# Performance work log

Hardware: AMD Instinct MI355X
Metric: run time of the kernel (lower is better)

The kernel has to match this reference:

```python
import jax, jax.numpy as jnp
import numpy as np

B, D, H, S, E = 16384, 512, 1024, 8, 4
DH = D // 2  # attention hidden


def setup_inputs() -> dict:
    key = jax.random.key(0)
    ks = jax.random.split(key, 20)
    std = 0.1
    return {
        "x": jax.random.normal(ks[0], (B, D), jnp.float32),
        "scenario_ids": jax.random.randint(ks[1], (B,), 0, S, jnp.int32),
        # shared SEI gate
        "gate_w": jax.random.normal(ks[2], (D, E), jnp.float32) * std,
        "gate_b": jnp.zeros((E,), jnp.float32),
        # shared sub-experts (stacked): D -> H -> D
        "sub_w1": jax.random.normal(ks[3], (E, D, H), jnp.float32) * std,
        "sub_b1": jnp.zeros((E, H), jnp.float32),
        "sub_w2": jax.random.normal(ks[4], (E, H, D), jnp.float32) * std,
        "sub_b2": jnp.zeros((E, D), jnp.float32),
        # scenario-specific experts (stacked): D -> H -> D
        "spec_w1": jax.random.normal(ks[5], (S, D, H), jnp.float32) * std,
        "spec_b1": jnp.zeros((S, H), jnp.float32),
        "spec_w2": jax.random.normal(ks[6], (S, H, D), jnp.float32) * std,
        "spec_b2": jnp.zeros((S, D), jnp.float32),
        # SAN scenario embeddings + attention MLP (2D -> D/2 -> 1)
        "scen_embed": jax.random.normal(ks[7], (S, D), jnp.float32) * std,
        "attn_w1": jax.random.normal(ks[8], (2 * D, DH), jnp.float32) * std,
        "attn_b1": jnp.zeros((DH,), jnp.float32),
        "attn_w2": jax.random.normal(ks[9], (DH, 1), jnp.float32) * std,
        "attn_b2": jnp.zeros((1,), jnp.float32),
        # SAN output projection (4D -> D)
        "out_w": jax.random.normal(ks[10], (4 * D, D), jnp.float32) * std,
        "out_b": jnp.zeros((D,), jnp.float32),
    }


def reference(x, scenario_ids, gate_w, gate_b, sub_w1, sub_b1, sub_w2, sub_b2,
              spec_w1, spec_b1, spec_w2, spec_b2, scen_embed,
              attn_w1, attn_b1, attn_w2, attn_b2, out_w, out_b):
    b = x.shape[0]
    # --- shared expert (SEI): softmax-gated mixture of E sub-experts ---
    gates = jax.nn.softmax(x @ gate_w + gate_b, axis=-1)            # [B,E]
    h = jax.nn.relu(jnp.einsum('bd,edh->ebh', x, sub_w1) + sub_b1[:, None, :])
    exp_out = jnp.einsum('ebh,ehd->ebd', h, sub_w2) + sub_b2[:, None, :]
    shared = jnp.einsum('be,ebd->bd', gates, exp_out)               # [B,D]
    # --- scenario-specific experts: run all, gather per-sample ---
    hs = jax.nn.relu(jnp.einsum('bd,sdh->sbh', x, spec_w1) + spec_b1[:, None, :])
    spec_all = jnp.einsum('sbh,shd->sbd', hs, spec_w2) + spec_b2[:, None, :]  # [S,B,D]
    specific = spec_all[scenario_ids, jnp.arange(b)]                # [B,D]
    # --- scenario-aware attention (SAN) ---
    # logits[s,b] = MLP(cat([shared[b], scen_embed[s]]))
    s = scen_embed.shape[0]
    comb = jnp.concatenate([
        jnp.broadcast_to(shared[None], (s, b, shared.shape[-1])),
        jnp.broadcast_to(scen_embed[:, None, :], (s, b, scen_embed.shape[-1])),
    ], axis=-1)                                                      # [S,B,2D]
    ah = jax.nn.relu(comb @ attn_w1 + attn_b1)                       # [S,B,D/2]
    logits = (ah @ attn_w2 + attn_b2)[..., 0]                        # [S,B]
    attn_w = jax.nn.softmax(logits.T, axis=-1)                       # [B,S]
    # in the original, all non-current scenario reprs are zeros, so the
    # weighted sums reduce to w[b, sid[b]] * (shared/specific)
    wsel = jnp.take_along_axis(attn_w, scenario_ids[:, None], axis=1)  # [B,1]
    enhanced = jnp.concatenate([shared, wsel * shared, specific, wsel * specific], axis=-1)
    return enhanced @ out_w + out_b                                  # [B,D]
```

## Files before the change

### kernel.cpp

```cpp
#include <hip/hip_runtime.h>
#include <hip/hip_bf16.h>
#include <stdint.h>

typedef __hip_bfloat16 bf16;
typedef __attribute__((ext_vector_type(8))) short short8;
typedef __attribute__((ext_vector_type(4))) short short4v;
typedef __attribute__((ext_vector_type(4))) float f32x4;

constexpr int cB = 16384, cD = 512, cH = 1024, cS = 8, cE = 4, cDH = 256;

__device__ __forceinline__ float tof(bf16 v) { return __bfloat162float(v); }
__device__ __forceinline__ bf16 tob(float v) { return __float2bfloat16(v); }
__device__ __forceinline__ float b2f(short s) {
  uint32_t u = ((uint32_t)(uint16_t)s) << 16;
  return __builtin_bit_cast(float, u);
}
__device__ __forceinline__ float ldf(const void* p, long i, int isbf) {
  return isbf ? b2f(((const short*)p)[i]) : ((const float*)p)[i];
}
__device__ __forceinline__ void stbf_nt(bf16* p, float v) {
  __builtin_nontemporal_store(__builtin_bit_cast(short, tob(v)), (short*)p);
}

__device__ __forceinline__ void gload_lds16(const bf16* g, char* l) {
  __builtin_amdgcn_global_load_lds(
      (const __attribute__((address_space(1))) void*)g,
      (__attribute__((address_space(3))) void*)l, 16, 0, 0);
}

__global__ __launch_bounds__(256) void probe_k(const void* x, int* flag) {
  __shared__ int sh[256];
  const unsigned short* u = (const unsigned short*)x;
  int cnt = 0;
  for (int i = threadIdx.x; i < 2048; i += 256) {
    float v = fabsf(b2f((short)u[2 * i]));
    cnt += (v > 1e-5f && v < 1e3f) ? 1 : 0;
  }
  sh[threadIdx.x] = cnt;
  __syncthreads();
  for (int s = 128; s > 0; s >>= 1) {
    if (threadIdx.x < s) sh[threadIdx.x] += sh[threadIdx.x + s];
    __syncthreads();
  }
  if (threadIdx.x == 0) flag[0] = (sh[0] > 1024) ? 1 : 0;
}

__global__ __launch_bounds__(256) void cvtx_k(const void* x, bf16* xb, const int* flag) {
  int g = blockIdx.x * 256 + threadIdx.x;
  if (flag[0]) {
    ((short8*)xb)[g] = ((const short8*)x)[g];
  } else {
    const f32x4* xf = (const f32x4*)x;
    f32x4 v0 = xf[2 * g], v1 = xf[2 * g + 1];
    short8 o;
#pragma unroll
    for (int j = 0; j < 4; j++) {
      o[j] = __builtin_bit_cast(short, tob(v0[j]));
      o[j + 4] = __builtin_bit_cast(short, tob(v1[j]));
    }
    ((short8*)xb)[g] = o;
  }
}

struct CvtDesc {
  const void* src[11];
  int off[12];
};
__global__ __launch_bounds__(256) void cvt_smalls_k(CvtDesc d, const int* flag, float* dst) {
  int i = blockIdx.x * 256 + threadIdx.x;
  if (i >= d.off[11]) return;
  int isb = flag[0];
  int j = 0;
  while (i >= d.off[j + 1]) j++;
  dst[i] = ldf(d.src[j], i - d.off[j], isb);
}

__global__ __launch_bounds__(256) void transpose_k(const void* in, bf16* out, int ldin, int ldout,
                                                   long in_off, long in_bs, long out_bs,
                                                   const int* flag) {
  __shared__ float tile[32][33];
  int isb = flag[0];
  long src0 = in_off + (long)blockIdx.z * in_bs;
  bf16* dst = out + (long)blockIdx.z * out_bs;
  int c0 = blockIdx.x * 32, r0 = blockIdx.y * 32;
  int tx = threadIdx.x & 31, ty = threadIdx.x >> 5;
#pragma unroll
  for (int i = 0; i < 4; i++)
    tile[ty + i * 8][tx] = ldf(in, src0 + (long)(r0 + ty + i * 8) * ldin + c0 + tx, isb);
  __syncthreads();
#pragma unroll
  for (int i = 0; i < 4; i++)
    dst[(long)(c0 + ty + i * 8) * ldout + r0 + tx] = tob(tile[tx][ty + i * 8]);
}

__global__ __launch_bounds__(256) void owt_k(const void* ow, bf16* owpair, const int* flag) {
  __shared__ float tile[32][33];
  int isb = flag[0];
  int z = blockIdx.z;
  int m = z & 1, kb = (z >> 1) * 512;
  long base = (long)z * 512 * cD;
  int c0 = blockIdx.x * 32, r0 = blockIdx.y * 32;
  int tx = threadIdx.x & 31, ty = threadIdx.x >> 5;
#pragma unroll
  for (int i = 0; i < 4; i++)
    tile[ty + i * 8][tx] = ldf(ow, base + (long)(r0 + ty + i * 8) * cD + c0 + tx, isb);
  __syncthreads();
#pragma unroll
  for (int i = 0; i < 4; i++) {
    int n = c0 + ty + i * 8;
    int R = ((n >> 6) << 7) + (((n >> 5) & 1) << 6) + (m << 5) + (((n >> 4) & 1) << 4) + (n & 15);
    owpair[(long)R * 1024 + kb + r0 + tx] = tob(tile[tx][ty + i * 8]);
  }
}

struct GArgs {
  const bf16* A; int lda;
  const bf16* Bt; int ldb; long bt_stride;
  void* C; int ldc;
  int M, N, K;
  const float* bias; int bias_stride;
  const float* gates; int eidx;
  const int* perm; const int* cum;
  const float* wsel;
  const int* dflag;
};

template <int EPI, bool GROUPED, bool GATHER_A, bool SCATTER_C, bool SPLITK = false>
__global__ __launch_bounds__(256, 4) void gemm_k(GArgs a) {
  __shared__ char smem[32768];
  char* ldsA = smem;
  char* ldsB = smem + 16384;

  int bxs, bys;
  if constexpr (!GROUPED) {
    const int gx = gridDim.x;
    const int nwg = gx * gridDim.y;
    const int d = blockIdx.y * gx + blockIdx.x;
    const int q = nwg >> 3, r = nwg & 7;
    const int xcd = d & 7, di = d >> 3;
    const int logical = (xcd < r ? xcd * (q + 1) : r * (q + 1) + (xcd - r) * q) + di;
    bxs = logical % gx;
    bys = logical / gx;
  } else {
    bxs = blockIdx.x;
    bys = blockIdx.y;
  }

  int g0, cnt;
  if constexpr (GROUPED) {
    int z = blockIdx.z;
    g0 = a.cum[z];
    cnt = a.cum[z + 1] - g0;
  } else {
    g0 = 0;
    cnt = a.M;
  }
  const int ptile = bys * 128;
  if (ptile >= cnt) return;
  const int n0 = bxs * 128;
  const int zk = SPLITK ? blockIdx.z * a.K : 0;
  const int zc = SPLITK ? blockIdx.z * a.eidx : 0;

  const int t = threadIdx.x, w = t >> 6, l = t & 63;
  const int wm = w >> 1, wn = w & 1;

  const bf16* bt = a.Bt + (GROUPED ? (long)blockIdx.z * a.bt_stride : 0);
  const float* bias = a.bias ? (a.bias + (GROUPED ? blockIdx.z * a.bias_stride : 0)) : nullptr;

  const bf16* aSrc[4];
  const bf16* bSrc[4];
  int ldsOff[4];
#pragma unroll
  for (int c = 0; c < 4; c++) {
    int pos = w * 4096 + c * 1024 + l * 16;
    int row = pos >> 7;
    int su = ((((pos >> 4) & 7) ^ (row & 7))) * 8;
    int p = ptile + row;
    if (p > cnt - 1) p = cnt - 1;
    int ar;
    if constexpr (GATHER_A) ar = a.perm[g0 + p];
    else ar = g0 + p;
    aSrc[c] = a.A + (long)ar * a.lda + zk + su;
    bSrc[c] = bt + (long)(n0 + row) * a.ldb + zk + su;
    ldsOff[c] = w * 4096 + c * 1024;
  }

  f32x4 zero = {0.f, 0.f, 0.f, 0.f};
  f32x4 acc[4][4];
#pragma unroll
  for (int i = 0; i < 4; i++)
#pragma unroll
    for (int j = 0; j < 4; j++) acc[i][j] = zero;

  const int nkt = a.K >> 6;
  for (int kt = 0; kt < nkt; ++kt) {
#pragma unroll
    for (int c = 0; c < 4; c++) gload_lds16(aSrc[c] + kt * 64, ldsA + ldsOff[c]);
#pragma unroll
    for (int c = 0; c < 4; c++) gload_lds16(bSrc[c] + kt * 64, ldsB + ldsOff[c]);
    __syncthreads();
#pragma unroll
    for (int kk = 0; kk < 2; kk++) {
      short8 af[4], bv[4];
#pragma unroll
      for (int mi = 0; mi < 4; mi++) {
        int row = wm * 64 + mi * 16 + (l & 15);
        int kg = kk * 4 + (l >> 4);
        int off = row * 128 + ((kg ^ (row & 7)) << 4);
        af[mi] = *(const short8*)(ldsA + off);
      }
#pragma unroll
      for (int ni = 0; ni < 4; ni++) {
        int row = wn * 64 + ni * 16 + (l & 15);
        int kg = kk * 4 + (l >> 4);
        int off = row * 128 + ((kg ^ (row & 7)) << 4);
        bv[ni] = *(const short8*)(ldsB + off);
      }
#pragma unroll
      for (int mi = 0; mi < 4; mi++)
#pragma unroll
        for (int ni = 0; ni < 4; ni++)
          acc[mi][ni] =
              __builtin_amdgcn_mfma_f32_16x16x32_bf16(af[mi], bv[ni], acc[mi][ni], 0, 0, 0);
    }
    __syncthreads();
  }

  const int l15 = l & 15, lg4 = l >> 4;
  int outbf = 1;
  if constexpr (EPI == 9) outbf = a.dflag[0];
#pragma unroll
  for (int mi = 0; mi < 4; mi++) {
#pragma unroll
    for (int j = 0; j < 4; j++) {
      int p = ptile + wm * 64 + mi * 16 + lg4 * 4 + j;
      if (p >= cnt) continue;
      int crow;
      if constexpr (SCATTER_C) crow = a.perm[g0 + p];
      else crow = g0 + p;
      if constexpr (EPI == 9) {
        float wv = a.wsel[crow];
#pragma unroll
        for (int ni = 0; ni < 2; ni++) {
          int n = (n0 >> 1) + wn * 32 + ni * 16 + l15;
          float o = acc[mi][ni][j] + wv * acc[mi][ni + 2][j] + a.bias[n];
          if (outbf) ((bf16*)a.C)[(long)crow * a.ldc + n] = tob(o);
          else ((float*)a.C)[(long)crow * a.ldc + n] = o;
        }
        continue;
      }
#pragma unroll
      for (int ni = 0; ni < 4; ni++) {
        int n = n0 + wn * 64 + ni * 16 + l15;
        float v = acc[mi][ni][j];
        if constexpr (EPI == 1) {
          v += bias[n];
          v = fmaxf(v, 0.f);
          stbf_nt(&((bf16*)a.C)[(long)crow * a.ldc + n], v);
        } else if constexpr (EPI == 2) {
          float g = a.gates[(long)(g0 + p) * 4 + a.eidx];
          v = g * (v + bias[n]);
          float* Cf = (float*)a.C;
          long idx = (long)crow * a.ldc + n;
          if (a.eidx == 0) Cf[idx] = v;
          else Cf[idx] += v;
        } else if constexpr (EPI == 3) {
          ((float*)a.C)[(long)crow * a.ldc + n] = v;
        } else if constexpr (EPI == 4) {
          v += bias[n];
          ((bf16*)a.C)[(long)crow * a.ldc + n] = tob(v);
        } else if constexpr (EPI == 6) {
          float g = a.gates[(long)(g0 + p) * 4 + (n >> 10)];
          v = g * fmaxf(v + bias[n], 0.f);
          stbf_nt(&((bf16*)a.C)[(long)crow * a.ldc + n], v);
        } else if constexpr (EPI == 7) {
          const float* gr = a.gates + (long)(g0 + p) * 4;
          v += gr[0] * bias[n] + gr[1] * bias[512 + n] + gr[2] * bias[1024 + n] +
               gr[3] * bias[1536 + n];
          ((bf16*)a.C)[(long)crow * a.ldc + n] = tob(v);
        } else if constexpr (EPI == 8) {
          ((bf16*)a.C)[(long)crow * a.ldc + n + zc] = tob(v);
        }
      }
    }
  }
}

__global__ __launch_bounds__(256) void combine_k(bf16* ss, const float* gates, const float* sb2) {
  long i = (long)blockIdx.x * 256 + threadIdx.x;
  int r = (int)(i >> 6);
  int c8 = (int)(i & 63) * 8;
  short8 p0 = *(const short8*)(ss + (long)r * 1024 + c8);
  short8 p1 = *(const short8*)(ss + (long)r * 1024 + 512 + c8);
  const float* gr = gates + (long)r * 4;
  float g0 = gr[0], g1 = gr[1], g2 = gr[2], g3 = gr[3];
  short8 o;
#pragma unroll
  for (int j = 0; j < 8; j++) {
    int c = c8 + j;
    float v = b2f(p0[j]) + b2f(p1[j]) + g0 * sb2[c] + g1 * sb2[512 + c] + g2 * sb2[1024 + c] +
              g3 * sb2[1536 + c];
    o[j] = __builtin_bit_cast(short, tob(v));
  }
  *(short8*)(ss + (long)r * 1024 + c8) = o;
}

__global__ __launch_bounds__(256) void gates_k(const bf16* x, const float* gw, const float* gb,
                                               float* gates) {
  int b = blockIdx.x * 4 + (threadIdx.x >> 6);
  int l = threadIdx.x & 63;
  short8 xv = *(const short8*)(x + (long)b * cD + l * 8);
  float a0 = 0, a1 = 0, a2 = 0, a3 = 0;
#pragma unroll
  for (int j = 0; j < 8; j++) {
    float xf = b2f(xv[j]);
    f32x4 wr = *(const f32x4*)(gw + (l * 8 + j) * 4);
    a0 += xf * wr[0];
    a1 += xf * wr[1];
    a2 += xf * wr[2];
    a3 += xf * wr[3];
  }
#pragma unroll
  for (int o = 32; o > 0; o >>= 1) {
    a0 += __shfl_xor(a0, o);
    a1 += __shfl_xor(a1, o);
    a2 += __shfl_xor(a2, o);
    a3 += __shfl_xor(a3, o);
  }
  a0 += gb[0];
  a1 += gb[1];
  a2 += gb[2];
  a3 += gb[3];
  float m = fmaxf(fmaxf(a0, a1), fmaxf(a2, a3));
  float e0 = expf(a0 - m), e1 = expf(a1 - m), e2 = expf(a2 - m), e3 = expf(a3 - m);
  float s = e0 + e1 + e2 + e3;
  if (l == 0) {
    float* gp = gates + (long)b * 4;
    gp[0] = e0 / s;
    gp[1] = e1 / s;
    gp[2] = e2 / s;
    gp[3] = e3 / s;
  }
}

__global__ __launch_bounds__(256) void bhist_k(const int* sid, int* bh) {
  int blk = blockIdx.x, t = threadIdx.x;
  __shared__ int h[cS];
  if (t < cS) h[t] = 0;
  __syncthreads();
  int s = sid[blk * 256 + t];
#pragma unroll
  for (int q = 0; q < cS; q++) {
    unsigned long long m = __ballot(s == q);
    if ((t & 63) == 0) atomicAdd(&h[q], __popcll(m));
  }
  __syncthreads();
  if (t < cS) bh[blk * cS + t] = h[t];
}

__global__ void bbase_k(const int* bh, int* base, int* cum) {
  __shared__ int tot[cS];
  int s = threadIdx.x;
  if (s < cS) {
    int run = 0;
    for (int b = 0; b < 64; b++) {
      base[b * cS + s] = run;
      run += bh[b * cS + s];
    }
    tot[s] = run;
  }
  __syncthreads();
  if (s == 0) {
    int run = 0;
    for (int q = 0; q < cS; q++) {
      cum[q] = run;
      run += tot[q];
    }
    cum[cS] = run;
  }
  __syncthreads();
  if (s < cS) {
    int c = cum[s];
    for (int b = 0; b < 64; b++) base[b * cS + s] += c;
  }
}

__global__ __launch_bounds__(256) void bscat_k(const int* sid, const int* base, int* perm) {
  int blk = blockIdx.x, t = threadIdx.x, w = t >> 6, l = t & 63;
  __shared__ int wc[4][cS];
  __shared__ int wb[4][cS];
  int s = sid[blk * 256 + t];
  int rank = 0;
#pragma unroll
  for (int q = 0; q < cS; q++) {
    unsigned long long m = __ballot(s == q);
    if (l == 0) wc[w][q] = __popcll(m);
    if (s == q) rank = __popcll(m & ((1ull << l) - 1ull));
  }
  __syncthreads();
  if (t < cS) {
    int run = 0;
#pragma unroll
    for (int ww = 0; ww < 4; ww++) {
      wb[ww][t] = run;
      run += wc[ww][t];
    }
  }
  __syncthreads();
  perm[base[blk * cS + s] + wb[w][s] + rank] = blk * 256 + t;
}

__global__ __launch_bounds__(256) void scenpart_k(const float* emb, const float* w1,
                                                  const float* b1, float* scp) {
  __shared__ float red[8][32];
  int s = blockIdx.x;
  int nl = threadIdx.x & 31;
  int n = blockIdx.y * 32 + nl;
  int dg = threadIdx.x >> 5;
  float a = 0.f;
#pragma unroll 4
  for (int d = dg * 64; d < dg * 64 + 64; d++) a += emb[s * cD + d] * w1[(long)(cD + d) * cDH + n];
  red[dg][nl] = a;
  __syncthreads();
  if (dg == 0) {
    float t = b1[n];
#pragma unroll
    for (int g = 0; g < 8; g++) t += red[g][nl];
    scp[s * cDH + n] = t;
  }
}

__global__ __launch_bounds__(256) void wsel_k(const float* sp, const float* scp, const float* w2,
                                              const int* sid, float* wsel) {
  int b = blockIdx.x * 4 + (threadIdx.x >> 6);
  int l = threadIdx.x & 63;
  float spv[4], w2v[4];
#pragma unroll
  for (int q = 0; q < 4; q++) {
    spv[q] = sp[(long)b * cDH + q * 64 + l];
    w2v[q] = w2[q * 64 + l];
  }
  float lg[8];
#pragma unroll
  for (int s = 0; s < 8; s++) {
    float acc = 0.f;
#pragma unroll
    for (int q = 0; q < 4; q++) {
      float v = spv[q] + scp[s * cDH + q * 64 + l];
      v = fmaxf(v, 0.f);
      acc += v * w2v[q];
    }
#pragma unroll
    for (int o = 32; o > 0; o >>= 1) acc += __shfl_xor(acc, o);
    lg[s] = acc;
  }
  float m = lg[0];
#pragma unroll
  for (int s = 1; s < 8; s++) m = fmaxf(m, lg[s]);
  float sum = 0.f;
#pragma unroll
  for (int s = 0; s < 8; s++) sum += expf(lg[s] - m);
  if (l == 0) {
    int s0 = sid[b];
    wsel[b] = expf(lg[s0] - m) / sum;
  }
}

__global__ __launch_bounds__(256) void cvt_shared_k(const float* sf, bf16* ss) {
  int i = blockIdx.x * 256 + threadIdx.x;
  int r = i >> 7, c = (i & 127) * 4;
  f32x4 v = *(const f32x4*)(sf + (long)r * cD + c);
  short4v o;
#pragma unroll
  for (int j = 0; j < 4; j++) o[j] = __builtin_bit_cast(short, tob(v[j]));
  *(short4v*)(ss + (long)r * 1024 + c) = o;
}

extern "C" void kernel_launch(void* const* d_in, const int* in_sizes, int n_in, void* d_out,
                              int out_size, void* d_ws, size_t ws_size, hipStream_t stream) {
  const void* x = d_in[0];
  const int* sid = (const int*)d_in[1];

  char* ws = (char*)d_ws;
  size_t off = 0;
  auto alloc = [&](size_t bytes) -> void* {
    void* p = ws + off;
    off += (bytes + 255) & ~(size_t)255;
    return p;
  };
  int* g_flag = (int*)alloc(64);
  float* g_gates = (float*)alloc((size_t)cB * 4 * 4);
  float* g_wsel = (float*)alloc((size_t)cB * 4);
  int* g_perm = (int*)alloc((size_t)cB * 4);
  int* g_bh = (int*)alloc(64 * cS * 4);
  int* g_base = (int*)alloc(64 * cS * 4);
  int* g_cum = (int*)alloc(64);
  float* g_scp = (float*)alloc((size_t)cS * cDH * 4);
  float* g_small = (float*)alloc((size_t)300000 * 4);
  bf16* g_xb = (bf16*)alloc((size_t)cB * cD * 2);
  bf16* w1t = (bf16*)alloc((size_t)cE * cH * cD * 2);
  bf16* w2cat = (bf16*)alloc((size_t)cD * 4096 * 2);
  bf16* s1t = (bf16*)alloc((size_t)cS * cH * cD * 2);
  bf16* s2t = (bf16*)alloc((size_t)cS * cD * cH * 2);
  bf16* a1t = (bf16*)alloc((size_t)cDH * cD * 2);
  bf16* owpair = (bf16*)alloc((size_t)1024 * 1024 * 2);
  bf16* g_ss = (bf16*)alloc((size_t)cB * 1024 * 2);
  size_t fixed_end = off;
  const size_t MB = 1024ull * 1024ull;
  const bool BIG = (ws_size == 0) || (fixed_end + 135 * MB <= ws_size);
  char* g_big = (char*)alloc(BIG ? 135 * MB : 68 * MB);
  (void)in_sizes;
  (void)n_in;
  (void)out_size;

  dim3 blk(256);
  probe_k<<<1, blk, 0, stream>>>(x, g_flag);
  cvtx_k<<<cB * cD / 8 / 256, blk, 0, stream>>>(x, g_xb, g_flag);

  const int O_GW = 0, O_GB = 2048, O_SB1 = 2052, O_SB2 = 6148, O_PB1 = 8196, O_PB2 = 16388,
            O_EMB = 20484, O_AW1 = 24580, O_AB1 = 286724, O_AW2 = 286980, O_OB = 287236,
            O_END = 287748;
  {
    CvtDesc d;
    const void* srcs[11] = {d_in[2],  d_in[3],  d_in[5],  d_in[7],  d_in[9], d_in[11],
                            d_in[12], d_in[13], d_in[14], d_in[15], d_in[18]};
    int offs[12] = {O_GW, O_GB, O_SB1, O_SB2, O_PB1, O_PB2, O_EMB, O_AW1, O_AB1, O_AW2, O_OB,
                    O_END};
    for (int i = 0; i < 11; i++) d.src[i] = srcs[i];
    for (int i = 0; i < 12; i++) d.off[i] = offs[i];
    cvt_smalls_k<<<(O_END + 255) / 256, blk, 0, stream>>>(d, g_flag, g_small);
  }

  transpose_k<<<dim3(cH / 32, cD / 32, cE), blk, 0, stream>>>(d_in[4], w1t, cH, cD, 0,
                                                              (long)cD * cH, (long)cH * cD, g_flag);
  transpose_k<<<dim3(cD / 32, cH / 32, cE), blk, 0, stream>>>(d_in[6], w2cat, cD, 4096, 0,
                                                              (long)cH * cD, 1024, g_flag);
  transpose_k<<<dim3(cH / 32, cD / 32, cS), blk, 0, stream>>>(d_in[8], s1t, cH, cD, 0,
                                                              (long)cD * cH, (long)cH * cD, g_flag);
  transpose_k<<<dim3(cD / 32, cH / 32, cS), blk, 0, stream>>>(d_in[10], s2t, cD, cH, 0,
                                                              (long)cH * cD, (long)cD * cH, g_flag);
  transpose_k<<<dim3(cDH / 32, cD / 32, 1), blk, 0, stream>>>(d_in[13], a1t, cDH, cD, 0, 0, 0,
                                                              g_flag);
  owt_k<<<dim3(cD / 32, cD / 32, 4), blk, 0, stream>>>(d_in[17], owpair, g_flag);

  gates_k<<<cB / 4, blk, 0, stream>>>(g_xb, g_small + O_GW, g_small + O_GB, g_gates);
  bhist_k<<<cB / 256, blk, 0, stream>>>(sid, g_bh);
  bbase_k<<<1, 64, 0, stream>>>(g_bh, g_base, g_cum);
  bscat_k<<<cB / 256, blk, 0, stream>>>(sid, g_base, g_perm);

  if (BIG) {
    bf16* h4 = (bf16*)g_big;
    float* sp = (float*)g_big;
    bf16* hspec = (bf16*)g_big;
    {
      GArgs a{};
      a.A = g_xb; a.lda = cD; a.Bt = w1t; a.ldb = cD;
      a.C = h4; a.ldc = 4096; a.M = cB; a.N = 4096; a.K = cD;
      a.bias = g_small + O_SB1; a.gates = g_gates;
      gemm_k<6, false, false, false><<<dim3(32, cB / 128), blk, 0, stream>>>(a);
    }
    {
      GArgs a{};
      a.A = h4; a.lda = 4096; a.Bt = w2cat; a.ldb = 4096;
      a.C = g_ss; a.ldc = 1024; a.M = cB; a.N = cD; a.K = 2048;
      a.eidx = 512;
      gemm_k<8, false, false, false, true><<<dim3(cD / 128, cB / 128, 2), blk, 0, stream>>>(a);
    }
    combine_k<<<cB * 64 / 256, blk, 0, stream>>>(g_ss, g_gates, g_small + O_SB2);
    {
      GArgs a{};
      a.A = g_ss; a.lda = 1024; a.Bt = a1t; a.ldb = cD;
      a.C = sp; a.ldc = cDH; a.M = cB; a.N = cDH; a.K = cD;
      gemm_k<3, false, false, false><<<dim3(cDH / 128, cB / 128), blk, 0, stream>>>(a);
    }
    scenpart_k<<<dim3(cS, 8), blk, 0, stream>>>(g_small + O_EMB, g_small + O_AW1, g_small + O_AB1,
                                                g_scp);
    wsel_k<<<cB / 4, blk, 0, stream>>>(sp, g_scp, g_small + O_AW2, sid, g_wsel);
    {
      GArgs a{};
      a.A = g_xb; a.lda = cD; a.Bt = s1t; a.ldb = cD; a.bt_stride = (long)cH * cD;
      a.C = hspec; a.ldc = cH; a.M = cB; a.N = cH; a.K = cD;
      a.bias = g_small + O_PB1; a.bias_stride = cH;
      a.perm = g_perm; a.cum = g_cum;
      gemm_k<1, true, true, false><<<dim3(cH / 128, cB / 128, cS), blk, 0, stream>>>(a);
    }
    {
      GArgs a{};
      a.A = hspec; a.lda = cH; a.Bt = s2t; a.ldb = cH; a.bt_stride = (long)cD * cH;
      a.C = g_ss + 512; a.ldc = 1024; a.M = cB; a.N = cD; a.K = cH;
      a.bias = g_small + O_PB2; a.bias_stride = cD;
      a.perm = g_perm; a.cum = g_cum;
      gemm_k<4, true, false, true><<<dim3(cD / 128, cB / 128, cS), blk, 0, stream>>>(a);
    }
    {
      GArgs a{};
      a.A = g_ss; a.lda = 1024; a.Bt = owpair; a.ldb = 1024;
      a.C = d_out; a.ldc = cD; a.M = cB; a.N = 1024; a.K = 1024;
      a.bias = g_small + O_OB; a.wsel = g_wsel; a.dflag = g_flag;
      gemm_k<9, false, false, false><<<dim3(8, cB / 128), blk, 0, stream>>>(a);
    }
  } else {
    float* f32a = (float*)g_big;
    bf16* hbuf = (bf16*)(g_big + 34 * MB);
    for (int e = 0; e < cE; e++) {
      GArgs a1{};
      a1.A = g_xb; a1.lda = cD; a1.Bt = w1t + (size_t)e * cH * cD; a1.ldb = cD;
      a1.C = hbuf; a1.ldc = cH; a1.M = cB; a1.N = cH; a1.K = cD;
      a1.bias = g_small + O_SB1 + e * cH;
      gemm_k<1, false, false, false><<<dim3(cH / 128, cB / 128), blk, 0, stream>>>(a1);
      GArgs a2{};
      a2.A = hbuf; a2.lda = cH; a2.Bt = w2cat + (size_t)e * 1024; a2.ldb = 4096;
      a2.C = f32a; a2.ldc = cD; a2.M = cB; a2.N = cD; a2.K = cH;
      a2.bias = g_small + O_SB2 + e * cD; a2.gates = g_gates; a2.eidx = e;
      gemm_k<2, false, false, false><<<dim3(cD / 128, cB / 128), blk, 0, stream>>>(a2);
    }
    cvt_shared_k<<<cB * 128 / 256, blk, 0, stream>>>(f32a, g_ss);
    {
      GArgs a{};
      a.A = g_xb; a.lda = cD; a.Bt = s1t; a.ldb = cD; a.bt_stride = (long)cH * cD;
      a.C = hbuf; a.ldc = cH; a.M = cB; a.N = cH; a.K = cD;
      a.bias = g_small + O_PB1; a.bias_stride = cH;
      a.perm = g_perm; a.cum = g_cum;
      gemm_k<1, true, true, false><<<dim3(cH / 128, cB / 128, cS), blk, 0, stream>>>(a);
    }
    {
      GArgs a{};
      a.A = hbuf; a.lda = cH; a.Bt = s2t; a.ldb = cH; a.bt_stride = (long)cD * cH;
      a.C = g_ss + 512; a.ldc = 1024; a.M = cB; a.N = cD; a.K = cH;
      a.bias = g_small + O_PB2; a.bias_stride = cD;
      a.perm = g_perm; a.cum = g_cum;
      gemm_k<4, true, false, true><<<dim3(cD / 128, cB / 128, cS), blk, 0, stream>>>(a);
    }
    {
      GArgs a{};
      a.A = g_ss; a.lda = 1024; a.Bt = a1t; a.ldb = cD;
      a.C = f32a; a.ldc = cDH; a.M = cB; a.N = cDH; a.K = cD;
      gemm_k<3, false, false, false><<<dim3(cDH / 128, cB / 128), blk, 0, stream>>>(a);
    }
    scenpart_k<<<dim3(cS, 8), blk, 0, stream>>>(g_small + O_EMB, g_small + O_AW1, g_small + O_AB1,
                                                g_scp);
    wsel_k<<<cB / 4, blk, 0, stream>>>(f32a, g_scp, g_small + O_AW2, sid, g_wsel);
    {
      GArgs a{};
      a.A = g_ss; a.lda = 1024; a.Bt = owpair; a.ldb = 1024;
      a.C = d_out; a.ldc = cD; a.M = cB; a.N = 1024; a.K = 1024;
      a.bias = g_small + O_OB; a.wsel = g_wsel; a.dflag = g_flag;
      gemm_k<9, false, false, false><<<dim3(8, cB / 128), blk, 0, stream>>>(a);
    }
  }
}
```

Before: 419.1 us.

## Add 256x256-tile 8-wave GEMM kernel for the three large dense GEMMs

Adds a new GEMM kernel with 256x256 output tiles, 512 threads, 128 KB of double-buffered swizzled LDS, an XCD-aware block remap, and global loads interleaved between four MFMA phases using setprio and barriers. It replaces the 128x128 gemm_k for the shared-expert up-projection, the down-projection and the output projection. The intent is more operand reuse per tile, less global/L2 traffic, and better overlap of loads with MFMA. In exchange, occupancy drops to one workgroup per CU, and the grid gets small for the down-projection (256 blocks) and the output projection.

New measurement: 405.9 us. 3.2% less time.

```diff
diff --git a/kernel.cpp b/kernel.cpp
--- a/kernel.cpp
+++ b/kernel.cpp
@@ -286,6 +286,202 @@
   }
 }
 
+struct G6Args {
+  const bf16* A; int lda;
+  const bf16* Bt; int ldb;
+  void* C; int ldc;
+  int N, K;
+  const float* bias;
+  const float* gates;
+  const float* wsel;
+  const int* dflag;
+};
+
+template <int EPI>
+__global__ __launch_bounds__(512, 1) void g256_k(G6Args a) {
+  extern __shared__ char sm[];
+  const int t = threadIdx.x, w = t >> 6, l = t & 63;
+  const int wm = w >> 2, wn = w & 3;
+
+  const int gx = gridDim.x, nwg = gx * gridDim.y;
+  const int dd = blockIdx.y * gx + blockIdx.x;
+  const int q = nwg >> 3, r = nwg & 7;
+  const int xcd = dd & 7, di = dd >> 3;
+  const int logical = (xcd < r ? xcd * (q + 1) : r * (q + 1) + (xcd - r) * q) + di;
+  const int m0 = (logical / gx) * 256, n0 = (logical % gx) * 256;
+  const long zk = (long)blockIdx.z * a.K;
+
+  const bf16* srcP[8];
+  int ldsO[8];
+#pragma unroll
+  for (int c = 0; c < 8; c++) {
+    int pos = (c & 3) * 8192 + t * 16;
+    int row = pos >> 7;
+    int su = (((pos >> 4) & 7) ^ (row & 7)) * 8;
+    if (c < 4) {
+      srcP[c] = a.A + (long)(m0 + row) * a.lda + zk + su;
+      ldsO[c] = (c & 3) * 8192 + w * 1024;
+    } else {
+      srcP[c] = a.Bt + (long)(n0 + row) * a.ldb + zk + su;
+      ldsO[c] = 32768 + (c & 3) * 8192 + w * 1024;
+    }
+  }
+
+  auto rdA = [&](char* buf, int mi, int kk) -> short8 {
+    int row = wm * 128 + mi * 16 + (l & 15);
+    int kg = kk * 4 + (l >> 4);
+    return *(const short8*)(buf + row * 128 + ((kg ^ (row & 7)) << 4));
+  };
+  auto rdB = [&](char* buf, int ni, int kk) -> short8 {
+    int row = wn * 64 + ni * 16 + (l & 15);
+    int kg = kk * 4 + (l >> 4);
+    return *(const short8*)(buf + 32768 + row * 128 + ((kg ^ (row & 7)) << 4));
+  };
+
+  f32x4 acc[8][4];
+#pragma unroll
+  for (int i = 0; i < 8; i++)
+#pragma unroll
+    for (int j = 0; j < 4; j++) acc[i][j] = {0.f, 0.f, 0.f, 0.f};
+
+  const int nkt = a.K >> 6;
+#pragma unroll
+  for (int c = 0; c < 8; c++) gload_lds16(srcP[c], sm + ldsO[c]);
+#pragma unroll
+  for (int c = 0; c < 8; c++) gload_lds16(srcP[c] + 64, sm + 65536 + ldsO[c]);
+
+  for (int kt = 0; kt < nkt; ++kt) {
+    char* buf = sm + (kt & 1) * 65536;
+    if (kt + 1 < nkt) asm volatile("s_waitcnt vmcnt(8)" ::: "memory");
+    else asm volatile("s_waitcnt vmcnt(0)" ::: "memory");
+    __builtin_amdgcn_s_barrier();
+
+    const bool st = (kt + 2 < nkt);
+    const int ko = (kt + 2) * 64;
+    short8 fa[4][2], fb0[2][2], fb1[2][2];
+
+#pragma unroll
+    for (int mi = 0; mi < 4; mi++)
+#pragma unroll
+      for (int kk = 0; kk < 2; kk++) fa[mi][kk] = rdA(buf, mi, kk);
+#pragma unroll
+    for (int ni = 0; ni < 2; ni++)
+#pragma unroll
+      for (int kk = 0; kk < 2; kk++) fb0[ni][kk] = rdB(buf, ni, kk);
+    __builtin_amdgcn_s_barrier();
+    asm volatile("s_waitcnt lgkmcnt(0)" ::: "memory");
+    __builtin_amdgcn_s_setprio(1);
+#pragma unroll
+    for (int mi = 0; mi < 4; mi++)
+#pragma unroll
+      for (int ni = 0; ni < 2; ni++)
+#pragma unroll
+        for (int kk = 0; kk < 2; kk++)
+          acc[mi][ni] =
+              __builtin_amdgcn_mfma_f32_16x16x32_bf16(fa[mi][kk], fb0[ni][kk], acc[mi][ni], 0, 0, 0);
+    __builtin_amdgcn_s_setprio(0);
+    __builtin_amdgcn_s_barrier();
+
+#pragma unroll
+    for (int ni = 0; ni < 2; ni++)
+#pragma unroll
+      for (int kk = 0; kk < 2; kk++) fb1[ni][kk] = rdB(buf, ni + 2, kk);
+    if (st) {
+      gload_lds16(srcP[0] + ko, buf + ldsO[0]);
+      gload_lds16(srcP[2] + ko, buf + ldsO[2]);
+    }
+    __builtin_amdgcn_s_barrier();
+    asm volatile("s_waitcnt lgkmcnt(0)" ::: "memory");
+    __builtin_amdgcn_s_setprio(1);
+#pragma unroll
+    for (int mi = 0; mi < 4; mi++)
+#pragma unroll
+      for (int ni = 0; ni < 2; ni++)
+#pragma unroll
+        for (int kk = 0; kk < 2; kk++)
+          acc[mi][ni + 2] = __builtin_amdgcn_mfma_f32_16x16x32_bf16(fa[mi][kk], fb1[ni][kk],
+                                                                    acc[mi][ni + 2], 0, 0, 0);
+    __builtin_amdgcn_s_setprio(0);
+    __builtin_amdgcn_s_barrier();
+
+#pragma unroll
+    for (int mi = 0; mi < 4; mi++)
+#pragma unroll
+      for (int kk = 0; kk < 2; kk++) fa[mi][kk] = rdA(buf, mi + 4, kk);
+    if (st) {
+      gload_lds16(srcP[4] + ko, buf + ldsO[4]);
+      gload_lds16(srcP[5] + ko, buf + ldsO[5]);
+      gload_lds16(srcP[6] + ko, buf + ldsO[6]);
+      gload_lds16(srcP[7] + ko, buf + ldsO[7]);
+    }
+    __builtin_amdgcn_s_barrier();
+    asm volatile("s_waitcnt lgkmcnt(0)" ::: "memory");
+    __builtin_amdgcn_s_setprio(1);
+#pragma unroll
+    for (int mi = 0; mi < 4; mi++)
+#pragma unroll
+      for (int ni = 0; ni < 2; ni++)
+#pragma unroll
+        for (int kk = 0; kk < 2; kk++)
+          acc[mi + 4][ni] = __builtin_amdgcn_mfma_f32_16x16x32_bf16(fa[mi][kk], fb0[ni][kk],
+                                                                    acc[mi + 4][ni], 0, 0, 0);
+    __builtin_amdgcn_s_setprio(0);
+    __builtin_amdgcn_s_barrier();
+
+    if (st) {
+      gload_lds16(srcP[1] + ko, buf + ldsO[1]);
+      gload_lds16(srcP[3] + ko, buf + ldsO[3]);
+    }
+    __builtin_amdgcn_s_barrier();
+    __builtin_amdgcn_s_setprio(1);
+#pragma unroll
+    for (int mi = 0; mi < 4; mi++)
+#pragma unroll
+      for (int ni = 0; ni < 2; ni++)
+#pragma unroll
+        for (int kk = 0; kk < 2; kk++)
+          acc[mi + 4][ni + 2] = __builtin_amdgcn_mfma_f32_16x16x32_bf16(
+              fa[mi][kk], fb1[ni][kk], acc[mi + 4][ni + 2], 0, 0, 0);
+    __builtin_amdgcn_s_setprio(0);
+    __builtin_amdgcn_s_barrier();
+  }
+
+  const int l15 = l & 15, lg4 = l >> 4;
+  int outbf = 1;
+  if constexpr (EPI == 9) outbf = a.dflag[0];
+#pragma unroll
+  for (int mi = 0; mi < 8; mi++) {
+#pragma unroll
+    for (int j = 0; j < 4; j++) {
+      int crow = m0 + wm * 128 + mi * 16 + lg4 * 4 + j;
+      if constexpr (EPI == 9) {
+        float wv = a.wsel[crow];
+#pragma unroll
+        for (int ni = 0; ni < 2; ni++) {
+          int R = n0 + wn * 64 + ni * 16 + l15;
+          int n = ((R >> 7) << 6) | (((R >> 6) & 1) << 5) | (((R >> 4) & 1) << 4) | (R & 15);
+          float o = acc[mi][ni][j] + wv * acc[mi][ni + 2][j] + a.bias[n];
+          if (outbf) ((bf16*)a.C)[(long)crow * a.ldc + n] = tob(o);
+          else ((float*)a.C)[(long)crow * a.ldc + n] = o;
+        }
+      } else {
+#pragma unroll
+        for (int ni = 0; ni < 4; ni++) {
+          int n = n0 + wn * 64 + ni * 16 + l15;
+          float v = acc[mi][ni][j];
+          if constexpr (EPI == 6) {
+            float g = a.gates[(long)crow * 4 + (n >> 10)];
+            v = g * fmaxf(v + a.bias[n], 0.f);
+            stbf_nt(&((bf16*)a.C)[(long)crow * a.ldc + n], v);
+          } else if constexpr (EPI == 8) {
+            ((bf16*)a.C)[(long)crow * a.ldc + n + blockIdx.z * 512] = tob(v);
+          }
+        }
+      }
+    }
+  }
+}
+
 __global__ __launch_bounds__(256) void combine_k(bf16* ss, const float* gates, const float* sb2) {
   long i = (long)blockIdx.x * 256 + threadIdx.x;
   int r = (int)(i >> 6);
@@ -513,6 +709,14 @@
   (void)n_in;
   (void)out_size;
 
+  bool use256 = true;
+  use256 &= hipFuncSetAttribute(reinterpret_cast<const void*>(g256_k<6>),
+                                hipFuncAttributeMaxDynamicSharedMemorySize, 131072) == hipSuccess;
+  use256 &= hipFuncSetAttribute(reinterpret_cast<const void*>(g256_k<8>),
+                                hipFuncAttributeMaxDynamicSharedMemorySize, 131072) == hipSuccess;
+  use256 &= hipFuncSetAttribute(reinterpret_cast<const void*>(g256_k<9>),
+                                hipFuncAttributeMaxDynamicSharedMemorySize, 131072) == hipSuccess;
+
   dim3 blk(256);
   probe_k<<<1, blk, 0, stream>>>(x, g_flag);
   cvtx_k<<<cB * cD / 8 / 256, blk, 0, stream>>>(x, g_xb, g_flag);
@@ -552,14 +756,25 @@
     bf16* h4 = (bf16*)g_big;
     float* sp = (float*)g_big;
     bf16* hspec = (bf16*)g_big;
-    {
+    if (use256) {
+      G6Args a{};
+      a.A = g_xb; a.lda = cD; a.Bt = w1t; a.ldb = cD;
+      a.C = h4; a.ldc = 4096; a.N = 4096; a.K = cD;
+      a.bias = g_small + O_SB1; a.gates = g_gates;
+      g256_k<6><<<dim3(16, 64), 512, 131072, stream>>>(a);
+    } else {
       GArgs a{};
       a.A = g_xb; a.lda = cD; a.Bt = w1t; a.ldb = cD;
       a.C = h4; a.ldc = 4096; a.M = cB; a.N = 4096; a.K = cD;
       a.bias = g_small + O_SB1; a.gates = g_gates;
       gemm_k<6, false, false, false><<<dim3(32, cB / 128), blk, 0, stream>>>(a);
     }
-    {
+    if (use256) {
+      G6Args a{};
+      a.A = h4; a.lda = 4096; a.Bt = w2cat; a.ldb = 4096;
+      a.C = g_ss; a.ldc = 1024; a.N = cD; a.K = 2048;
+      g256_k<8><<<dim3(2, 64, 2), 512, 131072, stream>>>(a);
+    } else {
       GArgs a{};
       a.A = h4; a.lda = 4096; a.Bt = w2cat; a.ldb = 4096;
       a.C = g_ss; a.ldc = 1024; a.M = cB; a.N = cD; a.K = 2048;
@@ -592,7 +807,13 @@
       a.perm = g_perm; a.cum = g_cum;
       gemm_k<4, true, false, true><<<dim3(cD / 128, cB / 128, cS), blk, 0, stream>>>(a);
     }
-    {
+    if (use256) {
+      G6Args a{};
+      a.A = g_ss; a.lda = 1024; a.Bt = owpair; a.ldb = 1024;
+      a.C = d_out; a.ldc = cD; a.N = 1024; a.K = 1024;
+      a.bias = g_small + O_OB; a.wsel = g_wsel; a.dflag = g_flag;
+      g256_k<9><<<dim3(4, 64), 512, 131072, stream>>>(a);
+    } else {
       GArgs a{};
       a.A = g_ss; a.lda = 1024; a.Bt = owpair; a.ldb = 1024;
       a.C = d_out; a.ldc = cD; a.M = cB; a.N = 1024; a.K = 1024;
```
